# Performance work log

Measured on AMD Instinct MI355X. Metric: run time of the kernel, lower is better.

Reference implementation:

```python
import jax, jax.numpy as jnp
import numpy as np

OBS_DIM, ACT_DIM, LATENT_DIM, BELIEF_DIM, T = 128, 32, 512, 1024, 32768


def setup_inputs() -> dict:
    key = jax.random.key(0)
    ks = jax.random.split(key, 8)
    s_ih = 1.0 / np.sqrt(BELIEF_DIM)
    s_enc = 1.0 / np.sqrt(OBS_DIM)
    return {
        "obs_seq": jax.random.normal(ks[0], (T, OBS_DIM), jnp.float32),
        "act_seq": jax.random.normal(ks[1], (T, ACT_DIM), jnp.float32),
        "enc_w": jax.random.uniform(ks[2], (LATENT_DIM, OBS_DIM), jnp.float32, -s_enc, s_enc),
        "enc_b": jax.random.uniform(ks[3], (LATENT_DIM,), jnp.float32, -s_enc, s_enc),
        "w_ih": jax.random.uniform(ks[4], (3 * BELIEF_DIM, LATENT_DIM + ACT_DIM), jnp.float32, -s_ih, s_ih),
        "w_hh": jax.random.uniform(ks[5], (3 * BELIEF_DIM, BELIEF_DIM), jnp.float32, -s_ih, s_ih),
        "b_ih": jax.random.uniform(ks[6], (3 * BELIEF_DIM,), jnp.float32, -s_ih, s_ih),
        "b_hh": jax.random.uniform(ks[7], (3 * BELIEF_DIM,), jnp.float32, -s_ih, s_ih),
    }


def reference(obs_seq, act_seq, enc_w, enc_b, w_ih, w_hh, b_ih, b_hh):
    H = w_hh.shape[1]
    # Encoder over all timesteps at once: (T, latent)
    z_seq = jnp.tanh(obs_seq @ enc_w.T + enc_b)
    # a_prev[t] = act_seq[t-1], zeros at t=0
    a_prev = jnp.concatenate(
        [jnp.zeros((1, act_seq.shape[1]), act_seq.dtype), act_seq[:-1]], axis=0)
    x_seq = jnp.concatenate([z_seq, a_prev], axis=-1)  # (T, latent+act)
    # Precompute input-side gate projections as one big GEMM: (T, 3H)
    gi_seq = x_seq @ w_ih.T + b_ih

    def step(h, gi_t):
        gh = w_hh @ h + b_hh  # (3H,)
        ir, iz, inn = jnp.split(gi_t, 3)
        hr, hz, hn = jnp.split(gh, 3)
        r = jax.nn.sigmoid(ir + hr)
        z = jax.nn.sigmoid(iz + hz)
        n = jnp.tanh(inn + r * hn)
        h_new = (1.0 - z) * n + z * h
        return h_new, h_new

    h0 = jnp.zeros((H,), x_seq.dtype)
    _, beliefs = jax.lax.scan(step, h0, gi_seq)
    return beliefs  # (T, belief_dim)
```

## Files before the change

### kernel.cpp

```cpp
#include <hip/hip_runtime.h>
#include <stdint.h>

#define T_STEPS 32768
#define HDIM    1024
#define LDIM    512
#define ADIM    32
#define NWG     128
#define NOUT    8

__device__ __forceinline__ float fast_sigmoid(float x) {
    float e = __expf(-x);
    return __builtin_amdgcn_rcpf(1.0f + e);
}
__device__ __forceinline__ float fast_tanh(float x) {
    float e = __expf(2.0f * x);
    return 1.0f - 2.0f * __builtin_amdgcn_rcpf(1.0f + e);
}

__global__ __launch_bounds__(256) void encoder_kernel(
    const float* __restrict__ obs,
    const float* __restrict__ w,
    const float* __restrict__ b,
    float* __restrict__ z)
{
    __shared__ float As[64][65];
    __shared__ float Bs[64][65];

    const int tile_n = blockIdx.x;
    const int tile_t = blockIdx.y;
    const int tid = threadIdx.x;
    const int ty = tid >> 4;
    const int tx = tid & 15;

    float acc[4][4] = {};

    for (int kt = 0; kt < 2; ++kt) {
        #pragma unroll
        for (int it = 0; it < 4; ++it) {
            int lin = it * 1024 + tid * 4;
            int r = lin >> 6, c = lin & 63;
            float4 va = *(const float4*)&obs[(size_t)(tile_t * 64 + r) * 128 + kt * 64 + c];
            As[r][c] = va.x; As[r][c+1] = va.y; As[r][c+2] = va.z; As[r][c+3] = va.w;
            float4 vb = *(const float4*)&w[(size_t)(tile_n * 64 + r) * 128 + kt * 64 + c];
            Bs[r][c] = vb.x; Bs[r][c+1] = vb.y; Bs[r][c+2] = vb.z; Bs[r][c+3] = vb.w;
        }
        __syncthreads();

        for (int k = 0; k < 64; ++k) {
            float av[4], bv[4];
            #pragma unroll
            for (int a = 0; a < 4; ++a) av[a] = As[ty * 4 + a][k];
            #pragma unroll
            for (int c = 0; c < 4; ++c) bv[c] = Bs[tx * 4 + c][k];
            #pragma unroll
            for (int a = 0; a < 4; ++a)
                #pragma unroll
                for (int c = 0; c < 4; ++c)
                    acc[a][c] = fmaf(av[a], bv[c], acc[a][c]);
        }
        __syncthreads();
    }

    #pragma unroll
    for (int a = 0; a < 4; ++a) {
        int row = tile_t * 64 + ty * 4 + a;
        #pragma unroll
        for (int c = 0; c < 4; ++c) {
            int col = tile_n * 64 + tx * 4 + c;
            z[(size_t)row * LDIM + col] = tanhf(acc[a][c] + b[col]);
        }
    }
}

__global__ __launch_bounds__(256, 1) void gru_kernel(
    float* __restrict__ out,
    const float* __restrict__ z_seq,
    const float* __restrict__ act,
    const float* __restrict__ w_ih,
    const float* __restrict__ w_hh,
    const float* __restrict__ b_ih,
    const float* __restrict__ b_hh,
    uint64_t* __restrict__ hbuf)
{
    __shared__ float h_lds[HDIM];
    __shared__ float z_lds[LDIM];
    __shared__ float a_lds[ADIM];
    __shared__ float h_pub[NOUT];

    const int tid  = threadIdx.x;
    const int wg   = blockIdx.x;
    const int grp  = tid >> 5;
    const int lane = tid & 31;
    const int i    = wg * NOUT + grp;

    float whr[32], whz[32], whn[32];
    {
        const float* pr = &w_hh[(size_t)i * HDIM + lane];
        const float* pz = &w_hh[(size_t)(HDIM + i) * HDIM + lane];
        const float* pn = &w_hh[(size_t)(2 * HDIM + i) * HDIM + lane];
        #pragma unroll
        for (int j = 0; j < 32; ++j) {
            whr[j] = pr[32 * j]; whz[j] = pz[32 * j]; whn[j] = pn[32 * j];
        }
    }
    float wir[17], wiz[17], win[17];
    {
        const float* pr = &w_ih[(size_t)i * 544 + lane];
        const float* pz = &w_ih[(size_t)(HDIM + i) * 544 + lane];
        const float* pn = &w_ih[(size_t)(2 * HDIM + i) * 544 + lane];
        #pragma unroll
        for (int j = 0; j < 17; ++j) {
            wir[j] = pr[32 * j]; wiz[j] = pz[32 * j]; win[j] = pn[32 * j];
        }
    }
    #pragma unroll
    for (int j = 0; j < 32; ++j) {
        asm volatile("" : "+v"(whr[j]), "+v"(whz[j]), "+v"(whn[j]));
    }
    #pragma unroll
    for (int j = 0; j < 17; ++j) {
        asm volatile("" : "+v"(wir[j]), "+v"(wiz[j]), "+v"(win[j]));
    }

    const float bias_r = b_ih[i] + b_hh[i];
    const float bias_z = b_ih[HDIM + i] + b_hh[HDIM + i];
    const float bin_   = b_ih[2 * HDIM + i];
    const float bhn    = b_hh[2 * HDIM + i];

    for (int q = tid; q < HDIM; q += 256) h_lds[q] = 0.0f;
    float hold = 0.0f;
    __syncthreads();

    for (int t = 0; t < T_STEPS; ++t) {
        if (tid < 128) {
            float4 v = *(const float4*)&z_seq[(size_t)t * LDIM + tid * 4];
            *(float4*)&z_lds[tid * 4] = v;
            if (tid < ADIM) {
                a_lds[tid] = (t == 0) ? 0.0f : act[(size_t)(t - 1) * ADIM + tid];
            }
        } else if (t > 0) {
            const int q = tid - 128;
            const uint64_t* bp = hbuf + ((size_t)((t - 1) & 1)) * HDIM + q * 8;
            const uint32_t want = (uint32_t)t;
            uint64_t v[8];
            int done = 0;
            while (done != 0xFF) {
                #pragma unroll
                for (int k = 0; k < 8; ++k) {
                    if (!(done & (1 << k))) {
                        v[k] = __hip_atomic_load(bp + k, __ATOMIC_RELAXED,
                                                 __HIP_MEMORY_SCOPE_AGENT);
                    }
                }
                #pragma unroll
                for (int k = 0; k < 8; ++k) {
                    if (!(done & (1 << k)) && (uint32_t)(v[k] >> 32) == want)
                        done |= (1 << k);
                }
            }
            float4 h0, h1;
            h0.x = __uint_as_float((uint32_t)v[0]);
            h0.y = __uint_as_float((uint32_t)v[1]);
            h0.z = __uint_as_float((uint32_t)v[2]);
            h0.w = __uint_as_float((uint32_t)v[3]);
            h1.x = __uint_as_float((uint32_t)v[4]);
            h1.y = __uint_as_float((uint32_t)v[5]);
            h1.z = __uint_as_float((uint32_t)v[6]);
            h1.w = __uint_as_float((uint32_t)v[7]);
            *(float4*)&h_lds[q * 8]     = h0;
            *(float4*)&h_lds[q * 8 + 4] = h1;
        }
        __syncthreads();

        float sr = 0.f, sz = 0.f, sn = 0.f;
        #pragma unroll
        for (int j = 0; j < 32; ++j) {
            float hv = h_lds[lane + 32 * j];
            sr = fmaf(whr[j], hv, sr);
            sz = fmaf(whz[j], hv, sz);
            sn = fmaf(whn[j], hv, sn);
        }
        float gr = 0.f, gz = 0.f, gn = 0.f;
        #pragma unroll
        for (int j = 0; j < 16; ++j) {
            float xv = z_lds[lane + 32 * j];
            gr = fmaf(wir[j], xv, gr);
            gz = fmaf(wiz[j], xv, gz);
            gn = fmaf(win[j], xv, gn);
        }
        {
            float xa = a_lds[lane];
            gr = fmaf(wir[16], xa, gr);
            gz = fmaf(wiz[16], xa, gz);
            gn = fmaf(win[16], xa, gn);
        }

        float vr = sr + gr, vz = sz + gz;
        #pragma unroll
        for (int m = 16; m >= 1; m >>= 1) {
            vr += __shfl_xor(vr, m);
            vz += __shfl_xor(vz, m);
            sn += __shfl_xor(sn, m);
            gn += __shfl_xor(gn, m);
        }

        if (lane == 0) {
            float r    = fast_sigmoid(vr + bias_r);
            float zg   = fast_sigmoid(vz + bias_z);
            float n    = fast_tanh(gn + bin_ + r * (sn + bhn));
            float hnew = (1.0f - zg) * n + zg * hold;
            hold = hnew;
            h_pub[grp] = hnew;
        }
        __syncthreads();

        if (tid < NOUT) {
            uint64_t pk = ((uint64_t)(uint32_t)(t + 1) << 32) |
                          (uint64_t)__float_as_uint(h_pub[tid]);
            __hip_atomic_store(&hbuf[((size_t)(t & 1)) * HDIM + wg * NOUT + tid],
                               pk, __ATOMIC_RELAXED, __HIP_MEMORY_SCOPE_AGENT);
        } else if (tid == NOUT) {
            float4 o0 = *(const float4*)&h_pub[0];
            float4 o1 = *(const float4*)&h_pub[4];
            *(float4*)&out[(size_t)t * HDIM + wg * NOUT]     = o0;
            *(float4*)&out[(size_t)t * HDIM + wg * NOUT + 4] = o1;
        }
    }
}

extern "C" void kernel_launch(void* const* d_in, const int* in_sizes, int n_in,
                              void* d_out, int out_size, void* d_ws, size_t ws_size,
                              hipStream_t stream) {
    const float* obs   = (const float*)d_in[0];
    const float* act   = (const float*)d_in[1];
    const float* enc_w = (const float*)d_in[2];
    const float* enc_b = (const float*)d_in[3];
    const float* w_ih  = (const float*)d_in[4];
    const float* w_hh  = (const float*)d_in[5];
    const float* b_ih  = (const float*)d_in[6];
    const float* b_hh  = (const float*)d_in[7];
    float* out = (float*)d_out;

    uint64_t* hbuf  = (uint64_t*)d_ws;
    float*    z_seq = (float*)((char*)d_ws + 65536);

    hipMemsetAsync(hbuf, 0, 2 * HDIM * sizeof(uint64_t), stream);

    encoder_kernel<<<dim3(8, 512), 256, 0, stream>>>(obs, enc_w, enc_b, z_seq);

    void* args[] = {(void*)&out, (void*)&z_seq, (void*)&act, (void*)&w_ih,
                    (void*)&w_hh, (void*)&b_ih, (void*)&b_hh, (void*)&hbuf};
    hipLaunchCooperativeKernel((void*)gru_kernel, dim3(NWG), dim3(256),
                               args, 0, stream);
}
```

Baseline: 87.01 ms.

## Publish hidden state per wavefront directly, removing second block barrier per step

Each 64-lane wavefront now computes the gate nonlinearity on all lanes, gathers its sibling half's result with a shuffle, and publishes both values straight to the global exchange buffer. This removes the shared h_pub staging and the second __syncthreads per timestep. The exchange buffer is re-laid out so each wavefront's pair sits alone in a 64-byte slot, which avoids false sharing between writers. Consumers poll per pair and write into LDS as soon as each pair arrives. The cost is a larger workspace and more scattered polling loads.

```diff
diff --git a/kernel.cpp b/kernel.cpp
--- a/kernel.cpp
+++ b/kernel.cpp
@@ -85,12 +85,13 @@
     __shared__ float h_lds[HDIM];
     __shared__ float z_lds[LDIM];
     __shared__ float a_lds[ADIM];
-    __shared__ float h_pub[NOUT];
 
     const int tid  = threadIdx.x;
     const int wg   = blockIdx.x;
     const int grp  = tid >> 5;
     const int lane = tid & 31;
+    const int wv   = tid >> 6;
+    const int wl   = tid & 63;
     const int i    = wg * NOUT + grp;
 
     float whr[32], whz[32], whn[32];
@@ -140,35 +141,34 @@
             }
         } else if (t > 0) {
             const int q = tid - 128;
-            const uint64_t* bp = hbuf + ((size_t)((t - 1) & 1)) * HDIM + q * 8;
+            const uint64_t* bp = hbuf + ((size_t)((t - 1) & 1)) * (512 * 8)
+                                      + (size_t)q * (4 * 8);
             const uint32_t want = (uint32_t)t;
-            uint64_t v[8];
+            uint64_t v0[4], v1[4];
             int done = 0;
-            while (done != 0xFF) {
+            while (done != 0xF) {
                 #pragma unroll
-                for (int k = 0; k < 8; ++k) {
-                    if (!(done & (1 << k))) {
-                        v[k] = __hip_atomic_load(bp + k, __ATOMIC_RELAXED,
-                                                 __HIP_MEMORY_SCOPE_AGENT);
+                for (int w = 0; w < 4; ++w) {
+                    if (!(done & (1 << w))) {
+                        v0[w] = __hip_atomic_load(bp + w * 8 + 0, __ATOMIC_RELAXED,
+                                                  __HIP_MEMORY_SCOPE_AGENT);
+                        v1[w] = __hip_atomic_load(bp + w * 8 + 1, __ATOMIC_RELAXED,
+                                                  __HIP_MEMORY_SCOPE_AGENT);
                     }
                 }
                 #pragma unroll
-                for (int k = 0; k < 8; ++k) {
-                    if (!(done & (1 << k)) && (uint32_t)(v[k] >> 32) == want)
-                        done |= (1 << k);
+                for (int w = 0; w < 4; ++w) {
+                    if (!(done & (1 << w)) &&
+                        (uint32_t)(v0[w] >> 32) == want &&
+                        (uint32_t)(v1[w] >> 32) == want) {
+                        done |= (1 << w);
+                        float2 hp;
+                        hp.x = __uint_as_float((uint32_t)v0[w]);
+                        hp.y = __uint_as_float((uint32_t)v1[w]);
+                        *(float2*)&h_lds[q * 8 + 2 * w] = hp;
+                    }
                 }
             }
-            float4 h0, h1;
-            h0.x = __uint_as_float((uint32_t)v[0]);
-            h0.y = __uint_as_float((uint32_t)v[1]);
-            h0.z = __uint_as_float((uint32_t)v[2]);
-            h0.w = __uint_as_float((uint32_t)v[3]);
-            h1.x = __uint_as_float((uint32_t)v[4]);
-            h1.y = __uint_as_float((uint32_t)v[5]);
-            h1.z = __uint_as_float((uint32_t)v[6]);
-            h1.w = __uint_as_float((uint32_t)v[7]);
-            *(float4*)&h_lds[q * 8]     = h0;
-            *(float4*)&h_lds[q * 8 + 4] = h1;
         }
         __syncthreads();
 
@@ -204,26 +204,27 @@
             gn += __shfl_xor(gn, m);
         }
 
-        if (lane == 0) {
-            float r    = fast_sigmoid(vr + bias_r);
-            float zg   = fast_sigmoid(vz + bias_z);
-            float n    = fast_tanh(gn + bin_ + r * (sn + bhn));
-            float hnew = (1.0f - zg) * n + zg * hold;
-            hold = hnew;
-            h_pub[grp] = hnew;
-        }
-        __syncthreads();
-
-        if (tid < NOUT) {
-            uint64_t pk = ((uint64_t)(uint32_t)(t + 1) << 32) |
-                          (uint64_t)__float_as_uint(h_pub[tid]);
-            __hip_atomic_store(&hbuf[((size_t)(t & 1)) * HDIM + wg * NOUT + tid],
-                               pk, __ATOMIC_RELAXED, __HIP_MEMORY_SCOPE_AGENT);
-        } else if (tid == NOUT) {
-            float4 o0 = *(const float4*)&h_pub[0];
-            float4 o1 = *(const float4*)&h_pub[4];
-            *(float4*)&out[(size_t)t * HDIM + wg * NOUT]     = o0;
-            *(float4*)&out[(size_t)t * HDIM + wg * NOUT + 4] = o1;
+        float r    = fast_sigmoid(vr + bias_r);
+        float zg   = fast_sigmoid(vz + bias_z);
+        float n    = fast_tanh(gn + bin_ + r * (sn + bhn));
+        float hnew = (1.0f - zg) * n + zg * hold;
+        hold = hnew;
+
+        float sib = __shfl(hnew, 32);
+        if (wl == 0) {
+            uint64_t pk0 = ((uint64_t)(uint32_t)(t + 1) << 32) |
+                           (uint64_t)__float_as_uint(hnew);
+            uint64_t pk1 = ((uint64_t)(uint32_t)(t + 1) << 32) |
+                           (uint64_t)__float_as_uint(sib);
+            uint64_t* lp = hbuf + ((size_t)(t & 1)) * (512 * 8)
+                                + (size_t)(wg * 4 + wv) * 8;
+            __hip_atomic_store(lp + 0, pk0, __ATOMIC_RELAXED,
+                               __HIP_MEMORY_SCOPE_AGENT);
+            __hip_atomic_store(lp + 1, pk1, __ATOMIC_RELAXED,
+                               __HIP_MEMORY_SCOPE_AGENT);
+        } else if (wl == 4) {
+            float2 o; o.x = hnew; o.y = sib;
+            *(float2*)&out[(size_t)t * HDIM + wg * NOUT + 2 * wv] = o;
         }
     }
 }
@@ -242,14 +243,14 @@
     float* out = (float*)d_out;
 
     uint64_t* hbuf  = (uint64_t*)d_ws;
-    float*    z_seq = (float*)((char*)d_ws + 65536);
-
-    hipMemsetAsync(hbuf, 0, 2 * HDIM * sizeof(uint64_t), stream);
+    float*    z_seq = (float*)((char*)d_ws + 131072);
+
+    (void)hipMemsetAsync(hbuf, 0, 65536, stream);
 
     encoder_kernel<<<dim3(8, 512), 256, 0, stream>>>(obs, enc_w, enc_b, z_seq);
 
     void* args[] = {(void*)&out, (void*)&z_seq, (void*)&act, (void*)&w_ih,
                     (void*)&w_hh, (void*)&b_ih, (void*)&b_hh, (void*)&hbuf};
-    hipLaunchCooperativeKernel((void*)gru_kernel, dim3(NWG), dim3(256),
-                               args, 0, stream);
-}
+    (void)hipLaunchCooperativeKernel((void*)gru_kernel, dim3(NWG), dim3(256),
+                                     args, 0, stream);
+}
```

Result: slower. 110.5 ms (+27.0%).
